# Performance work log

Measured on AMD Instinct MI355X. Metric: run time of the kernel, lower is better.

## Reference

```python
import jax, jax.numpy as jnp
import numpy as np

N_QUBITS = 6
N_LAYERS = 4
N_ACTIONS = 4
PRE_DIM = 64
BATCH = 262144


def _cnot(state, ctrl, tgt):
    # state: (B, 2,...,2); flip target axis on the control=1 slice
    ca, ta = 1 + ctrl, 1 + tgt
    s0 = jnp.take(state, 0, axis=ca)
    s1 = jnp.take(state, 1, axis=ca)
    ta_in = ta if ta < ca else ta - 1
    s1 = jnp.flip(s1, axis=ta_in)
    return jnp.stack([s0, s1], axis=ca)


def _ry_batched(state, angles_q, q):
    # angles_q: (B,) per-sample RY angle on qubit q (AngleEmbedding)
    h = angles_q * 0.5
    c, s = jnp.cos(h), jnp.sin(h)
    R = jnp.stack([jnp.stack([c, -s], -1), jnp.stack([s, c], -1)], -2)  # (B,2,2)
    st = jnp.moveaxis(state, 1 + q, -1)
    st = jnp.einsum('b...i,bji->b...j', st, R)
    return jnp.moveaxis(st, -1, 1 + q)


def _ry_scalar(state, theta, q):
    h = theta * 0.5
    c, s = jnp.cos(h), jnp.sin(h)
    R = jnp.stack([jnp.stack([c, -s]), jnp.stack([s, c])])  # (2,2)
    st = jnp.moveaxis(state, 1 + q, -1)
    st = st @ R.T  # new_j = sum_i R[j,i] amp_i
    return jnp.moveaxis(st, -1, 1 + q)


def _circuit(xp, qw):
    # xp: (B, n_qubits) angles; qw: (n_layers, n_qubits)
    B = xp.shape[0]
    state = jnp.zeros((B,) + (2,) * N_QUBITS, xp.dtype)
    state = state.at[(slice(None),) + (0,) * N_QUBITS].set(1.0)
    for q in range(N_QUBITS):
        state = _ry_batched(state, xp[:, q], q)
    for l in range(N_LAYERS):
        for i in range(N_QUBITS):
            state = _cnot(state, i, (i + 1) % N_QUBITS)
        for i in range(N_QUBITS):
            state = _ry_scalar(state, qw[l, i], i)
    probs = state * state  # RY/CNOT are real; state stays real
    all_axes = tuple(range(1, N_QUBITS + 1))
    zs = []
    for q in range(N_QUBITS):
        p = jnp.sum(probs, axis=tuple(a for a in all_axes if a != 1 + q))  # (B,2)
        zs.append(p[:, 0] - p[:, 1])
    return jnp.stack(zs, -1)  # (B, n_qubits)


def setup_inputs() -> dict:
    key = jax.random.key(0)
    ks = jax.random.split(key, 10)
    x = jax.random.normal(ks[0], (BATCH, N_QUBITS), jnp.float32)
    sc = 1.0 / np.sqrt(N_QUBITS)
    W1 = jax.random.uniform(ks[1], (PRE_DIM, N_QUBITS), jnp.float32, -sc, sc)
    b1 = jax.random.uniform(ks[2], (PRE_DIM,), jnp.float32, -sc, sc)
    sc2 = 1.0 / np.sqrt(PRE_DIM)
    W2 = jax.random.uniform(ks[3], (N_QUBITS, PRE_DIM), jnp.float32, -sc2, sc2)
    b2 = jax.random.uniform(ks[4], (N_QUBITS,), jnp.float32, -sc2, sc2)
    qw = jax.random.uniform(ks[5], (N_LAYERS, N_QUBITS), jnp.float32, 0.0, 2.0 * np.pi)
    Wp = jax.random.uniform(ks[6], (N_ACTIONS, N_QUBITS), jnp.float32, -sc, sc)
    bp = jax.random.uniform(ks[7], (N_ACTIONS,), jnp.float32, -sc, sc)
    Wv = jax.random.uniform(ks[8], (1, N_QUBITS), jnp.float32, -sc, sc)
    bv = jax.random.uniform(ks[9], (1,), jnp.float32, -sc, sc)
    return {"x": x, "W1": W1, "b1": b1, "W2": W2, "b2": b2, "qw": qw,
            "Wp": Wp, "bp": bp, "Wv": Wv, "bv": bv}


def reference(x, W1, b1, W2, b2, qw, Wp, bp, Wv, bv):
    h = jax.nn.relu(x @ W1.T + b1)
    xp = jax.nn.relu(h @ W2.T + b2)          # (B, n_qubits)
    qout = _circuit(xp, qw)                   # (B, n_qubits)
    policy = jax.nn.softmax(qout @ Wp.T + bp, axis=-1)
    value = (qout @ Wv.T + bv)[:, 0]
    return policy, value
```

## Files before the change

### kernel.cpp

```cpp
#include <hip/hip_runtime.h>
#include <math.h>


#define NQ 6
#define NL 4
#define NA 4
#define PD 64

typedef float v2 __attribute__((ext_vector_type(2)));

__device__ __forceinline__ v2 mk2(float a, float b) { v2 r; r.x = a; r.y = b; return r; }
__device__ __forceinline__ v2 pkfma(v2 a, v2 b, v2 c) { return __builtin_elementwise_fma(a, b, c); }

__global__ __launch_bounds__(256) void qpolicy_kernel(
    const float* __restrict__ x,
    const float* __restrict__ W1,
    const float* __restrict__ b1,
    const float* __restrict__ W2,
    const float* __restrict__ b2,
    const float* __restrict__ qw,
    const float* __restrict__ Wp,
    const float* __restrict__ bp,
    const float* __restrict__ Wv,
    const float* __restrict__ bv,
    float* __restrict__ out,
    int B)
{
    const int tid = blockIdx.x * blockDim.x + threadIdx.x;

    const v2* xv = reinterpret_cast<const v2*>(x + (size_t)tid * NQ);
    const v2 x01 = xv[0], x23 = xv[1], x45 = xv[2];

    const v2* W1v = reinterpret_cast<const v2*>(W1);
    const v2* W2v = reinterpret_cast<const v2*>(W2);

    v2 h2[PD / 2];
#pragma unroll
    for (int j2 = 0; j2 < PD / 2; ++j2) {
        float hj[2];
#pragma unroll
        for (int u = 0; u < 2; ++u) {
            const int j = 2 * j2 + u;
            v2 acc = mk2(b1[j], 0.0f);
            acc = pkfma(x01, W1v[j * 3 + 0], acc);
            acc = pkfma(x23, W1v[j * 3 + 1], acc);
            acc = pkfma(x45, W1v[j * 3 + 2], acc);
            hj[u] = fmaxf(acc.x + acc.y, 0.0f);
        }
        h2[j2] = mk2(hj[0], hj[1]);
    }

    float xp[NQ];
#pragma unroll
    for (int i = 0; i < NQ; ++i) {
        v2 acc = mk2(b2[i], 0.0f);
#pragma unroll
        for (int k = 0; k < PD / 2; ++k) acc = pkfma(h2[k], W2v[i * (PD / 2) + k], acc);
        xp[i] = fmaxf(acc.x + acc.y, 0.0f);
    }

    float cq[NQ], sq[NQ];
#pragma unroll
    for (int q = 0; q < NQ; ++q) __sincosf(0.5f * xp[q], &sq[q], &cq[q]);

    float pr[32];
    pr[0] = 1.0f;
#pragma unroll
    for (int q = 0; q < 5; ++q) {
        const int sz = 1 << q;
#pragma unroll
        for (int k = sz - 1; k >= 0; --k) {
            const float v = pr[k];
            pr[2 * k]     = v * cq[q];
            pr[2 * k + 1] = v * sq[q];
        }
    }
    v2 st[32];
    const v2 cs5 = mk2(cq[5], sq[5]);
#pragma unroll
    for (int k = 0; k < 32; ++k) st[k] = mk2(pr[k], pr[k]) * cs5;

#pragma unroll
    for (int l = 0; l < NL; ++l) {
#pragma unroll
        for (int i = 0; i < 4; ++i) {
            const int mc = 1 << (4 - i), mt = 1 << (3 - i);
#pragma unroll
            for (int k = 0; k < 32; ++k) {
                if ((k & mc) && !(k & mt)) {
                    v2 tmp = st[k]; st[k] = st[k | mt]; st[k | mt] = tmp;
                }
            }
        }
#pragma unroll
        for (int k = 0; k < 32; ++k) {
            if (k & 1) st[k] = __builtin_shufflevector(st[k], st[k], 1, 0);
        }
#pragma unroll
        for (int k = 0; k < 16; ++k) {
            const float tmp = st[k].y; st[k].y = st[k | 16].y; st[k | 16].y = tmp;
        }

        float tv[NQ], sv[NQ];
#pragma unroll
        for (int i = 0; i < NQ; ++i) {
            float hh = 0.5f * qw[l * NQ + i];
            hh = (hh > 1.5707963f) ? (hh - 3.14159265358979f) : hh;
            float sh, ch;
            __sincosf(hh, &sh, &ch);
            sv[i] = sh;
            tv[i] = sh * __builtin_amdgcn_rcpf(1.0f + ch);
        }

#pragma unroll
        for (int i = 0; i < 5; ++i) {
            const int m = 1 << (4 - i);
            const v2 vnt = mk2(-tv[i], -tv[i]);
            const v2 vs  = mk2(sv[i], sv[i]);
#pragma unroll
            for (int k = 0; k < 32; ++k) {
                if (!(k & m)) {
                    v2 a = st[k], b = st[k | m];
                    a = pkfma(vnt, b, a);
                    b = pkfma(vs, a, b);
                    a = pkfma(vnt, b, a);
                    st[k] = a; st[k | m] = b;
                }
            }
        }
        {
            const float nt = -tv[5], s5 = sv[5];
#pragma unroll
            for (int k = 0; k < 32; ++k) {
                float a0 = st[k].x, a1 = st[k].y;
                a0 = fmaf(nt, a1, a0);
                a1 = fmaf(s5, a0, a1);
                a0 = fmaf(nt, a1, a0);
                st[k] = mk2(a0, a1);
            }
        }
    }

    float a[32];
    float S5 = 0.0f;
#pragma unroll
    for (int k = 0; k < 32; ++k) {
        const v2 p = st[k] * st[k];
        a[k] = p.x + p.y;
        S5 += p.x;
    }
    float S0 = 0.0f;
#pragma unroll
    for (int k = 0; k < 16; ++k) S0 += a[k];
    float b16[16];
#pragma unroll
    for (int k = 0; k < 16; ++k) b16[k] = a[k] + a[k | 16];
    float S1 = 0.0f;
#pragma unroll
    for (int k = 0; k < 8; ++k) S1 += b16[k];
    float b8[8];
#pragma unroll
    for (int k = 0; k < 8; ++k) b8[k] = b16[k] + b16[k | 8];
    const float S2 = b8[0] + b8[1] + b8[2] + b8[3];
    float b4[4];
#pragma unroll
    for (int k = 0; k < 4; ++k) b4[k] = b8[k] + b8[k | 4];
    const float S3 = b4[0] + b4[1];
    float b2a[2];
    b2a[0] = b4[0] + b4[2];
    b2a[1] = b4[1] + b4[3];
    const float S4 = b2a[0];
    const float T = b2a[0] + b2a[1];

    float z[NQ];
    z[0] = fmaf(2.0f, S0, -T);
    z[1] = fmaf(2.0f, S1, -T);
    z[2] = fmaf(2.0f, S2, -T);
    z[3] = fmaf(2.0f, S3, -T);
    z[4] = fmaf(2.0f, S4, -T);
    z[5] = fmaf(2.0f, S5, -T);

    float logits[NA];
#pragma unroll
    for (int aidx = 0; aidx < NA; ++aidx) {
        float acc = bp[aidx];
#pragma unroll
        for (int q = 0; q < NQ; ++q) acc = fmaf(z[q], Wp[aidx * NQ + q], acc);
        logits[aidx] = acc;
    }
    float m = logits[0];
#pragma unroll
    for (int aidx = 1; aidx < NA; ++aidx) m = fmaxf(m, logits[aidx]);
    float e[NA];
    float esum = 0.0f;
#pragma unroll
    for (int aidx = 0; aidx < NA; ++aidx) { e[aidx] = __expf(logits[aidx] - m); esum += e[aidx]; }
    const float inv = 1.0f / esum;

    float4 pol;
    pol.x = e[0] * inv; pol.y = e[1] * inv; pol.z = e[2] * inv; pol.w = e[3] * inv;
    reinterpret_cast<float4*>(out)[tid] = pol;

    float v = bv[0];
#pragma unroll
    for (int q = 0; q < NQ; ++q) v = fmaf(z[q], Wv[q], v);
    out[(size_t)B * NA + tid] = v;
}

extern "C" void kernel_launch(void* const* d_in, const int* in_sizes, int n_in,
                              void* d_out, int out_size, void* d_ws, size_t ws_size,
                              hipStream_t stream) {
    const float* x  = (const float*)d_in[0];
    const float* W1 = (const float*)d_in[1];
    const float* b1 = (const float*)d_in[2];
    const float* W2 = (const float*)d_in[3];
    const float* b2 = (const float*)d_in[4];
    const float* qw = (const float*)d_in[5];
    const float* Wp = (const float*)d_in[6];
    const float* bp = (const float*)d_in[7];
    const float* Wv = (const float*)d_in[8];
    const float* bv = (const float*)d_in[9];
    float* out = (float*)d_out;

    const int B = in_sizes[0] / NQ;
    dim3 block(256);
    dim3 grid((B + 255) / 256);
    hipLaunchKernelGGL(qpolicy_kernel, grid, block, 0, stream,
                       x, W1, b1, W2, b2, qw, Wp, bp, Wv, bv, out, B);
}
```

Measured before the change: 98.90 us.

## Precompute circuit unitary and apply it via split-bf16 MFMA matmul

The fixed-weight part of the circuit (CNOT and RY layers from qw) is folded into a 64x64 real unitary, built once by a small single-block kernel into workspace as hi/lo bf16 MFMA fragments. The main kernel builds each sample's product-state vector, stages it through LDS, and multiplies by the unitary using three bf16 MFMAs per tile (hi*hi, hi*lo, lo*hi) to approximate fp32 accuracy. It then squares the results and reduces them to Z expectations. This replaces the per-thread gate simulation with matrix-core work, at the cost of an extra launch, LDS round trips, and a small precision loss from the 3-term bf16 split. Each block now handles 512 samples over two iterations.

```diff
diff --git a/kernel.cpp b/kernel.cpp
--- a/kernel.cpp
+++ b/kernel.cpp
@@ -8,203 +8,287 @@
 #define PD 64
 
 typedef float v2 __attribute__((ext_vector_type(2)));
+using bf16x8 = __attribute__((ext_vector_type(8))) short;
+using f32x4  = __attribute__((ext_vector_type(4))) float;
 
 __device__ __forceinline__ v2 mk2(float a, float b) { v2 r; r.x = a; r.y = b; return r; }
 __device__ __forceinline__ v2 pkfma(v2 a, v2 b, v2 c) { return __builtin_elementwise_fma(a, b, c); }
 
-__global__ __launch_bounds__(256) void qpolicy_kernel(
+__device__ __forceinline__ void split2(float f0, float f1, unsigned int& hi, unsigned int& lo) {
+    unsigned int u0 = __float_as_uint(f0), u1 = __float_as_uint(f1);
+    unsigned int h0 = u0 & 0xFFFF0000u, h1 = u1 & 0xFFFF0000u;
+    hi = (u0 >> 16) | h1;
+    float l0 = f0 - __uint_as_float(h0);
+    float l1 = f1 - __uint_as_float(h1);
+    lo = (__float_as_uint(l0) >> 16) | (__float_as_uint(l1) & 0xFFFF0000u);
+}
+
+__device__ __forceinline__ bf16x8 as_bf16x8(uint4 u) {
+    union { uint4 a; bf16x8 b; } c; c.a = u; return c.b;
+}
+
+__global__ __launch_bounds__(64) void build_u_kernel(
+    const float* __restrict__ qw, uint4* __restrict__ ufrag)
+{
+    __shared__ float Ut[64 * 68];
+    const int e = threadIdx.x;
+
+    float st[64];
+#pragma unroll
+    for (int k = 0; k < 64; ++k) st[k] = (k == e) ? 1.0f : 0.0f;
+
+#pragma unroll
+    for (int l = 0; l < NL; ++l) {
+#pragma unroll
+        for (int i = 0; i < NQ; ++i) {
+            const int cm = 1 << (5 - i), tm = 1 << (5 - ((i + 1) % NQ));
+#pragma unroll
+            for (int idx = 0; idx < 64; ++idx) {
+                if ((idx & cm) && !(idx & tm)) {
+                    float t = st[idx]; st[idx] = st[idx | tm]; st[idx | tm] = t;
+                }
+            }
+        }
+#pragma unroll
+        for (int i = 0; i < NQ; ++i) {
+            const int qm = 1 << (5 - i);
+            float sh, ch;
+            sincosf(0.5f * qw[l * NQ + i], &sh, &ch);
+#pragma unroll
+            for (int idx = 0; idx < 64; ++idx) {
+                if (!(idx & qm)) {
+                    float a0 = st[idx], a1 = st[idx | qm];
+                    st[idx]      = ch * a0 - sh * a1;
+                    st[idx | qm] = ch * a1 + sh * a0;
+                }
+            }
+        }
+    }
+
+#pragma unroll
+    for (int j = 0; j < 64; ++j) Ut[j * 68 + e] = st[j];
+    __syncthreads();
+
+    const int c = e & 15, q = e >> 4;
+#pragma unroll
+    for (int f = 0; f < 8; ++f) {
+        const int nt = f >> 1, kb = f & 1;
+        float v[8];
+#pragma unroll
+        for (int j = 0; j < 8; ++j)
+            v[j] = Ut[(16 * nt + c) * 68 + 32 * kb + 8 * q + j];
+        uint4 hi, lo;
+        split2(v[0], v[1], hi.x, lo.x);
+        split2(v[2], v[3], hi.y, lo.y);
+        split2(v[4], v[5], hi.z, lo.z);
+        split2(v[6], v[7], hi.w, lo.w);
+        ufrag[f * 64 + e]       = hi;
+        ufrag[512 + f * 64 + e] = lo;
+    }
+}
+
+#define WREG 18432
+
+__global__ __launch_bounds__(256, 2) void qpolicy_mfma(
     const float* __restrict__ x,
     const float* __restrict__ W1,
     const float* __restrict__ b1,
     const float* __restrict__ W2,
     const float* __restrict__ b2,
-    const float* __restrict__ qw,
     const float* __restrict__ Wp,
     const float* __restrict__ bp,
     const float* __restrict__ Wv,
     const float* __restrict__ bv,
+    const uint4* __restrict__ ufrag,
     float* __restrict__ out,
     int B)
 {
-    const int tid = blockIdx.x * blockDim.x + threadIdx.x;
-
-    const v2* xv = reinterpret_cast<const v2*>(x + (size_t)tid * NQ);
-    const v2 x01 = xv[0], x23 = xv[1], x45 = xv[2];
+    __shared__ __align__(16) unsigned char smem[4 * WREG];
+    const int lane = threadIdx.x & 63;
+    const int wave = threadIdx.x >> 6;
+    unsigned char* Ahi = smem + wave * WREG;
+    unsigned char* Alo = Ahi + 9216;
+
+    bf16x8 Uh[8], Ul[8];
+#pragma unroll
+    for (int f = 0; f < 8; ++f) {
+        Uh[f] = as_bf16x8(ufrag[f * 64 + lane]);
+        Ul[f] = as_bf16x8(ufrag[512 + f * 64 + lane]);
+    }
 
     const v2* W1v = reinterpret_cast<const v2*>(W1);
     const v2* W2v = reinterpret_cast<const v2*>(W2);
-
-    v2 h2[PD / 2];
-#pragma unroll
-    for (int j2 = 0; j2 < PD / 2; ++j2) {
-        float hj[2];
-#pragma unroll
-        for (int u = 0; u < 2; ++u) {
-            const int j = 2 * j2 + u;
-            v2 acc = mk2(b1[j], 0.0f);
-            acc = pkfma(x01, W1v[j * 3 + 0], acc);
-            acc = pkfma(x23, W1v[j * 3 + 1], acc);
-            acc = pkfma(x45, W1v[j * 3 + 2], acc);
-            hj[u] = fmaxf(acc.x + acc.y, 0.0f);
-        }
-        h2[j2] = mk2(hj[0], hj[1]);
+    const int c15 = lane & 15, q4 = lane >> 4;
+
+#pragma unroll 1
+    for (int it = 0; it < 2; ++it) {
+        const int elem = blockIdx.x * 512 + it * 256 + (int)threadIdx.x;
+
+        const v2* xv = reinterpret_cast<const v2*>(x + (size_t)elem * NQ);
+        const v2 x01 = xv[0], x23 = xv[1], x45 = xv[2];
+
+        v2 h2[PD / 2];
+#pragma unroll
+        for (int j2 = 0; j2 < PD / 2; ++j2) {
+            float hj[2];
+#pragma unroll
+            for (int u = 0; u < 2; ++u) {
+                const int j = 2 * j2 + u;
+                v2 acc = mk2(b1[j], 0.0f);
+                acc = pkfma(x01, W1v[j * 3 + 0], acc);
+                acc = pkfma(x23, W1v[j * 3 + 1], acc);
+                acc = pkfma(x45, W1v[j * 3 + 2], acc);
+                hj[u] = fmaxf(acc.x + acc.y, 0.0f);
+            }
+            h2[j2] = mk2(hj[0], hj[1]);
+        }
+        float xp[NQ];
+#pragma unroll
+        for (int i = 0; i < NQ; ++i) {
+            v2 acc = mk2(b2[i], 0.0f);
+#pragma unroll
+            for (int k = 0; k < PD / 2; ++k) acc = pkfma(h2[k], W2v[i * (PD / 2) + k], acc);
+            xp[i] = fmaxf(acc.x + acc.y, 0.0f);
+        }
+
+        float cq[NQ], sq[NQ];
+#pragma unroll
+        for (int q = 0; q < NQ; ++q) __sincosf(0.5f * xp[q], &sq[q], &cq[q]);
+        float pr[64];
+        pr[0] = 1.0f;
+#pragma unroll
+        for (int q = 0; q < NQ; ++q) {
+            const int sz = 1 << q;
+#pragma unroll
+            for (int k = sz - 1; k >= 0; --k) {
+                const float v = pr[k];
+                pr[2 * k]     = v * cq[q];
+                pr[2 * k + 1] = v * sq[q];
+            }
+        }
+
+#pragma unroll
+        for (int w = 0; w < 8; ++w) {
+            uint4 hi, lo;
+            split2(pr[8 * w + 0], pr[8 * w + 1], hi.x, lo.x);
+            split2(pr[8 * w + 2], pr[8 * w + 3], hi.y, lo.y);
+            split2(pr[8 * w + 4], pr[8 * w + 5], hi.z, lo.z);
+            split2(pr[8 * w + 6], pr[8 * w + 7], hi.w, lo.w);
+            *reinterpret_cast<uint4*>(Ahi + lane * 144 + w * 16) = hi;
+            *reinterpret_cast<uint4*>(Alo + lane * 144 + w * 16) = lo;
+        }
+
+        bf16x8 Ah[4][2], Al[4][2];
+#pragma unroll
+        for (int mt = 0; mt < 4; ++mt)
+#pragma unroll
+            for (int kb = 0; kb < 2; ++kb) {
+                const int off = (16 * mt + c15) * 144 + kb * 64 + q4 * 16;
+                Ah[mt][kb] = *reinterpret_cast<const bf16x8*>(Ahi + off);
+                Al[mt][kb] = *reinterpret_cast<const bf16x8*>(Alo + off);
+            }
+
+        f32x4 C[4][4];
+#pragma unroll
+        for (int mt = 0; mt < 4; ++mt)
+#pragma unroll
+            for (int nt = 0; nt < 4; ++nt) C[mt][nt] = (f32x4){0.f, 0.f, 0.f, 0.f};
+#pragma unroll
+        for (int kb = 0; kb < 2; ++kb)
+#pragma unroll
+            for (int mt = 0; mt < 4; ++mt)
+#pragma unroll
+                for (int nt = 0; nt < 4; ++nt) {
+                    const int f = nt * 2 + kb;
+                    C[mt][nt] = __builtin_amdgcn_mfma_f32_16x16x32_bf16(Ah[mt][kb], Uh[f], C[mt][nt], 0, 0, 0);
+                    C[mt][nt] = __builtin_amdgcn_mfma_f32_16x16x32_bf16(Ah[mt][kb], Ul[f], C[mt][nt], 0, 0, 0);
+                    C[mt][nt] = __builtin_amdgcn_mfma_f32_16x16x32_bf16(Al[mt][kb], Uh[f], C[mt][nt], 0, 0, 0);
+                }
+
+#pragma unroll
+        for (int mt = 0; mt < 4; ++mt)
+#pragma unroll
+            for (int nt = 0; nt < 4; ++nt)
+#pragma unroll
+                for (int r = 0; r < 4; ++r) {
+                    const float vv = C[mt][nt][r];
+                    const int row = 16 * mt + 4 * q4 + r;
+                    const int col = 16 * nt + c15;
+                    *reinterpret_cast<float*>(Ahi + row * 272 + col * 4) = vv * vv;
+                }
+
+        float pv[64];
+#pragma unroll
+        for (int w = 0; w < 16; ++w) {
+            f32x4 t = *reinterpret_cast<const f32x4*>(Ahi + lane * 272 + w * 16);
+            pv[4 * w + 0] = t[0]; pv[4 * w + 1] = t[1];
+            pv[4 * w + 2] = t[2]; pv[4 * w + 3] = t[3];
+        }
+
+        float a32[32], S5 = 0.0f;
+#pragma unroll
+        for (int k = 0; k < 32; ++k) {
+            a32[k] = pv[2 * k] + pv[2 * k + 1];
+            S5 += pv[2 * k];
+        }
+        float S0 = 0.0f;
+#pragma unroll
+        for (int k = 0; k < 16; ++k) S0 += a32[k];
+        float b16[16];
+#pragma unroll
+        for (int k = 0; k < 16; ++k) b16[k] = a32[k] + a32[k | 16];
+        float S1 = 0.0f;
+#pragma unroll
+        for (int k = 0; k < 8; ++k) S1 += b16[k];
+        float b8[8];
+#pragma unroll
+        for (int k = 0; k < 8; ++k) b8[k] = b16[k] + b16[k | 8];
+        const float S2 = b8[0] + b8[1] + b8[2] + b8[3];
+        float b4[4];
+#pragma unroll
+        for (int k = 0; k < 4; ++k) b4[k] = b8[k] + b8[k | 4];
+        const float S3 = b4[0] + b4[1];
+        float b2a[2];
+        b2a[0] = b4[0] + b4[2];
+        b2a[1] = b4[1] + b4[3];
+        const float S4 = b2a[0];
+        const float T = b2a[0] + b2a[1];
+
+        float z[NQ];
+        z[0] = fmaf(2.0f, S0, -T);
+        z[1] = fmaf(2.0f, S1, -T);
+        z[2] = fmaf(2.0f, S2, -T);
+        z[3] = fmaf(2.0f, S3, -T);
+        z[4] = fmaf(2.0f, S4, -T);
+        z[5] = fmaf(2.0f, S5, -T);
+
+        float logits[NA];
+#pragma unroll
+        for (int aidx = 0; aidx < NA; ++aidx) {
+            float acc = bp[aidx];
+#pragma unroll
+            for (int q = 0; q < NQ; ++q) acc = fmaf(z[q], Wp[aidx * NQ + q], acc);
+            logits[aidx] = acc;
+        }
+        float m = logits[0];
+#pragma unroll
+        for (int aidx = 1; aidx < NA; ++aidx) m = fmaxf(m, logits[aidx]);
+        float e[NA], esum = 0.0f;
+#pragma unroll
+        for (int aidx = 0; aidx < NA; ++aidx) { e[aidx] = __expf(logits[aidx] - m); esum += e[aidx]; }
+        const float inv = 1.0f / esum;
+
+        if (elem < B) {
+            float4 pol;
+            pol.x = e[0] * inv; pol.y = e[1] * inv; pol.z = e[2] * inv; pol.w = e[3] * inv;
+            reinterpret_cast<float4*>(out)[elem] = pol;
+
+            float v = bv[0];
+#pragma unroll
+            for (int q = 0; q < NQ; ++q) v = fmaf(z[q], Wv[q], v);
+            out[(size_t)B * NA + elem] = v;
+        }
     }
-
-    float xp[NQ];
-#pragma unroll
-    for (int i = 0; i < NQ; ++i) {
-        v2 acc = mk2(b2[i], 0.0f);
-#pragma unroll
-        for (int k = 0; k < PD / 2; ++k) acc = pkfma(h2[k], W2v[i * (PD / 2) + k], acc);
-        xp[i] = fmaxf(acc.x + acc.y, 0.0f);
-    }
-
-    float cq[NQ], sq[NQ];
-#pragma unroll
-    for (int q = 0; q < NQ; ++q) __sincosf(0.5f * xp[q], &sq[q], &cq[q]);
-
-    float pr[32];
-    pr[0] = 1.0f;
-#pragma unroll
-    for (int q = 0; q < 5; ++q) {
-        const int sz = 1 << q;
-#pragma unroll
-        for (int k = sz - 1; k >= 0; --k) {
-            const float v = pr[k];
-            pr[2 * k]     = v * cq[q];
-            pr[2 * k + 1] = v * sq[q];
-        }
-    }
-    v2 st[32];
-    const v2 cs5 = mk2(cq[5], sq[5]);
-#pragma unroll
-    for (int k = 0; k < 32; ++k) st[k] = mk2(pr[k], pr[k]) * cs5;
-
-#pragma unroll
-    for (int l = 0; l < NL; ++l) {
-#pragma unroll
-        for (int i = 0; i < 4; ++i) {
-            const int mc = 1 << (4 - i), mt = 1 << (3 - i);
-#pragma unroll
-            for (int k = 0; k < 32; ++k) {
-                if ((k & mc) && !(k & mt)) {
-                    v2 tmp = st[k]; st[k] = st[k | mt]; st[k | mt] = tmp;
-                }
-            }
-        }
-#pragma unroll
-        for (int k = 0; k < 32; ++k) {
-            if (k & 1) st[k] = __builtin_shufflevector(st[k], st[k], 1, 0);
-        }
-#pragma unroll
-        for (int k = 0; k < 16; ++k) {
-            const float tmp = st[k].y; st[k].y = st[k | 16].y; st[k | 16].y = tmp;
-        }
-
-        float tv[NQ], sv[NQ];
-#pragma unroll
-        for (int i = 0; i < NQ; ++i) {
-            float hh = 0.5f * qw[l * NQ + i];
-            hh = (hh > 1.5707963f) ? (hh - 3.14159265358979f) : hh;
-            float sh, ch;
-            __sincosf(hh, &sh, &ch);
-            sv[i] = sh;
-            tv[i] = sh * __builtin_amdgcn_rcpf(1.0f + ch);
-        }
-
-#pragma unroll
-        for (int i = 0; i < 5; ++i) {
-            const int m = 1 << (4 - i);
-            const v2 vnt = mk2(-tv[i], -tv[i]);
-            const v2 vs  = mk2(sv[i], sv[i]);
-#pragma unroll
-            for (int k = 0; k < 32; ++k) {
-                if (!(k & m)) {
-                    v2 a = st[k], b = st[k | m];
-                    a = pkfma(vnt, b, a);
-                    b = pkfma(vs, a, b);
-                    a = pkfma(vnt, b, a);
-                    st[k] = a; st[k | m] = b;
-                }
-            }
-        }
-        {
-            const float nt = -tv[5], s5 = sv[5];
-#pragma unroll
-            for (int k = 0; k < 32; ++k) {
-                float a0 = st[k].x, a1 = st[k].y;
-                a0 = fmaf(nt, a1, a0);
-                a1 = fmaf(s5, a0, a1);
-                a0 = fmaf(nt, a1, a0);
-                st[k] = mk2(a0, a1);
-            }
-        }
-    }
-
-    float a[32];
-    float S5 = 0.0f;
-#pragma unroll
-    for (int k = 0; k < 32; ++k) {
-        const v2 p = st[k] * st[k];
-        a[k] = p.x + p.y;
-        S5 += p.x;
-    }
-    float S0 = 0.0f;
-#pragma unroll
-    for (int k = 0; k < 16; ++k) S0 += a[k];
-    float b16[16];
-#pragma unroll
-    for (int k = 0; k < 16; ++k) b16[k] = a[k] + a[k | 16];
-    float S1 = 0.0f;
-#pragma unroll
-    for (int k = 0; k < 8; ++k) S1 += b16[k];
-    float b8[8];
-#pragma unroll
-    for (int k = 0; k < 8; ++k) b8[k] = b16[k] + b16[k | 8];
-    const float S2 = b8[0] + b8[1] + b8[2] + b8[3];
-    float b4[4];
-#pragma unroll
-    for (int k = 0; k < 4; ++k) b4[k] = b8[k] + b8[k | 4];
-    const float S3 = b4[0] + b4[1];
-    float b2a[2];
-    b2a[0] = b4[0] + b4[2];
-    b2a[1] = b4[1] + b4[3];
-    const float S4 = b2a[0];
-    const float T = b2a[0] + b2a[1];
-
-    float z[NQ];
-    z[0] = fmaf(2.0f, S0, -T);
-    z[1] = fmaf(2.0f, S1, -T);
-    z[2] = fmaf(2.0f, S2, -T);
-    z[3] = fmaf(2.0f, S3, -T);
-    z[4] = fmaf(2.0f, S4, -T);
-    z[5] = fmaf(2.0f, S5, -T);
-
-    float logits[NA];
-#pragma unroll
-    for (int aidx = 0; aidx < NA; ++aidx) {
-        float acc = bp[aidx];
-#pragma unroll
-        for (int q = 0; q < NQ; ++q) acc = fmaf(z[q], Wp[aidx * NQ + q], acc);
-        logits[aidx] = acc;
-    }
-    float m = logits[0];
-#pragma unroll
-    for (int aidx = 1; aidx < NA; ++aidx) m = fmaxf(m, logits[aidx]);
-    float e[NA];
-    float esum = 0.0f;
-#pragma unroll
-    for (int aidx = 0; aidx < NA; ++aidx) { e[aidx] = __expf(logits[aidx] - m); esum += e[aidx]; }
-    const float inv = 1.0f / esum;
-
-    float4 pol;
-    pol.x = e[0] * inv; pol.y = e[1] * inv; pol.z = e[2] * inv; pol.w = e[3] * inv;
-    reinterpret_cast<float4*>(out)[tid] = pol;
-
-    float v = bv[0];
-#pragma unroll
-    for (int q = 0; q < NQ; ++q) v = fmaf(z[q], Wv[q], v);
-    out[(size_t)B * NA + tid] = v;
 }
 
 extern "C" void kernel_launch(void* const* d_in, const int* in_sizes, int n_in,
@@ -223,8 +307,10 @@
     float* out = (float*)d_out;
 
     const int B = in_sizes[0] / NQ;
-    dim3 block(256);
-    dim3 grid((B + 255) / 256);
-    hipLaunchKernelGGL(qpolicy_kernel, grid, block, 0, stream,
-                       x, W1, b1, W2, b2, qw, Wp, bp, Wv, bv, out, B);
-}
+
+    hipLaunchKernelGGL(build_u_kernel, dim3(1), dim3(64), 0, stream,
+                       qw, (uint4*)d_ws);
+    hipLaunchKernelGGL(qpolicy_mfma, dim3((B + 511) / 512), dim3(256), 0, stream,
+                       x, W1, b1, W2, b2, Wp, bp, Wv, bv,
+                       (const uint4*)d_ws, out, B);
+}
```

Result: slower. 141.5 us (+43.1%).
